# Kernel optimization log

Measured on AMD Instinct MI355X. Metric: run time of the kernel, lower is better.

## Reference

```python
import jax, jax.numpy as jnp
import numpy as np

B, C, S = 32, 256, 64  # batch, channels, spatial_size (h == w == S)


def _xavier(key, shape):
    fan_in, fan_out = shape[0], shape[1]
    bound = float(np.sqrt(6.0 / (fan_in + fan_out)))
    return jax.random.uniform(key, shape, jnp.float32, -bound, bound)


def setup_inputs() -> dict:
    key = jax.random.key(0)
    ks = jax.random.split(key, 7)
    x = jax.random.normal(ks[0], (B, C, S, S), dtype=jnp.float32)
    ww0 = _xavier(ks[1], (S, 1))
    ww1 = _xavier(ks[2], (S, 1))
    ww2 = _xavier(ks[3], (S, 1))
    hw0 = _xavier(ks[4], (S, 1))
    hw1 = _xavier(ks[5], (S, 1))
    hw2 = _xavier(ks[6], (S, 1))
    z = jnp.zeros((1, S), dtype=jnp.float32)
    return {
        'x': x,
        'ww0': ww0, 'ww1': ww1, 'ww2': ww2,
        'wb0': z, 'wb1': z, 'wb2': z,
        'hw0': hw0, 'hw1': hw1, 'hw2': hw2,
        'hb0': z, 'hb1': z, 'hb2': z,
    }


def _branch(mean_vec, max_vec, w0, w1, w2, b0, b1, b2):
    # mean_vec, max_vec: (b, S); w*: (S, 1); b*: (1, S)
    s = jax.nn.softmax(mean_vec, axis=1)          # (b, S)
    y0 = mean_vec @ w0                            # (b, 1)
    y1 = max_vec @ w1                             # (b, 1)
    y0_t = jnp.tanh(y0 * s + b0)                  # (b, S)
    y1_t = jnp.tanh(y1 * s + b1)                  # (b, S)
    return (y1_t @ w2) * y0_t + b2                # (b, S)


def reference(x, ww0, ww1, ww2, wb0, wb1, wb2, hw0, hw1, hw2, hb0, hb1, hb2):
    # x: (b, c, h, w) with h == w == S
    sp_max = jnp.max(x, axis=1)                   # (b, h, w)
    sp_mean = jnp.mean(x, axis=1)                 # (b, h, w)
    width_max = jnp.max(sp_max, axis=1)           # (b, w)
    width_mean = jnp.mean(sp_mean, axis=1)        # (b, w)
    height_max = jnp.max(sp_max, axis=2)          # (b, h)
    height_mean = jnp.mean(sp_mean, axis=2)       # (b, h)
    y_w = _branch(width_mean, width_max, ww0, ww1, ww2, wb0, wb1, wb2)   # (b, w)
    y_h = _branch(height_mean, height_max, hw0, hw1, hw2, hb0, hb1, hb2)  # (b, h)
    spatial = jnp.tanh(y_h[:, :, None] * y_w[:, None, :])[:, None]       # (b,1,h,w)
    return x * (spatial + 1.0)
```

## Files before the change

kernel.cpp:

```cpp
#include <hip/hip_runtime.h>
#include <float.h>

#define BB 32
#define CC 256
#define SS 64
#define IMG (SS * SS)
#define NPIX (BB * IMG)
#define NTOT (BB * CC * IMG)

__device__ __forceinline__ float4 f4max(float4 a, float4 b) {
    return make_float4(fmaxf(a.x, b.x), fmaxf(a.y, b.y), fmaxf(a.z, b.z), fmaxf(a.w, b.w));
}
__device__ __forceinline__ float4 f4add(float4 a, float4 b) {
    return make_float4(a.x + b.x, a.y + b.y, a.z + b.z, a.w + b.w);
}

__global__ __launch_bounds__(256) void reduce_c_kernel(const float* __restrict__ x,
                                                       float* __restrict__ sp_max,
                                                       float* __restrict__ sp_mean) {
    const int blk   = blockIdx.x;
    const int b     = blk >> 4;
    const int chunk = blk & 15;
    const int tid   = threadIdx.x;
    const int wave  = tid >> 6;
    const int lane  = tid & 63;
    const int pos   = (chunk << 8) + (lane << 2);

    const float* xp = x + ((size_t)(b * CC + wave * 64) << 12) + pos;

    float4 vmax = make_float4(-FLT_MAX, -FLT_MAX, -FLT_MAX, -FLT_MAX);
    float4 vsum = make_float4(0.f, 0.f, 0.f, 0.f);
#pragma unroll 8
    for (int c = 0; c < 64; ++c) {
        float4 v = *(const float4*)(xp + ((size_t)c << 12));
        vmax = f4max(vmax, v);
        vsum = f4add(vsum, v);
    }

    __shared__ float4 smax[4][64];
    __shared__ float4 ssum[4][64];
    smax[wave][lane] = vmax;
    ssum[wave][lane] = vsum;
    __syncthreads();

    if (wave == 0) {
        float4 m = smax[0][lane];
        float4 s = ssum[0][lane];
#pragma unroll
        for (int w = 1; w < 4; ++w) {
            m = f4max(m, smax[w][lane]);
            s = f4add(s, ssum[w][lane]);
        }
        const float inv = 1.0f / (float)CC;
        float4 mn = make_float4(s.x * inv, s.y * inv, s.z * inv, s.w * inv);
        *(float4*)(sp_max + (size_t)b * IMG + pos) = m;
        *(float4*)(sp_mean + (size_t)b * IMG + pos) = mn;
    }
}

__device__ __forceinline__ float allreduce_sum(float v) {
#pragma unroll
    for (int o = 32; o > 0; o >>= 1) v += __shfl_xor(v, o);
    return v;
}
__device__ __forceinline__ float allreduce_max(float v) {
#pragma unroll
    for (int o = 32; o > 0; o >>= 1) v = fmaxf(v, __shfl_xor(v, o));
    return v;
}

__device__ __forceinline__ float branch_lane(float meanv, float maxv,
                                             float w0, float w1, float w2,
                                             float b0, float b1, float b2) {
    float m  = allreduce_max(meanv);
    float e  = expf(meanv - m);
    float s  = e / allreduce_sum(e);
    float y0 = allreduce_sum(meanv * w0);
    float y1 = allreduce_sum(maxv * w1);
    float y0t = tanhf(fmaf(y0, s, b0));
    float y1t = tanhf(fmaf(y1, s, b1));
    float yw2 = allreduce_sum(y1t * w2);
    return fmaf(yw2, y0t, b2);
}

__global__ __launch_bounds__(64) void branch_kernel(
        const float* __restrict__ sp_max, const float* __restrict__ sp_mean,
        const float* __restrict__ ww0, const float* __restrict__ ww1, const float* __restrict__ ww2,
        const float* __restrict__ wb0, const float* __restrict__ wb1, const float* __restrict__ wb2,
        const float* __restrict__ hw0, const float* __restrict__ hw1, const float* __restrict__ hw2,
        const float* __restrict__ hb0, const float* __restrict__ hb1, const float* __restrict__ hb2,
        float* __restrict__ spatial) {
    const int b = blockIdx.x;
    const int t = threadIdx.x;
    const float* smx = sp_max + (size_t)b * IMG;
    const float* smn = sp_mean + (size_t)b * IMG;

    float wmax = -FLT_MAX, wsum = 0.f;
    float hmax = -FLT_MAX, hsum = 0.f;
#pragma unroll 4
    for (int i = 0; i < 64; ++i) {
        wmax = fmaxf(wmax, smx[i * 64 + t]);
        wsum += smn[i * 64 + t];
        hmax = fmaxf(hmax, smx[t * 64 + i]);
        hsum += smn[t * 64 + i];
    }
    const float inv = 1.0f / (float)SS;
    float y_w = branch_lane(wsum * inv, wmax, ww0[t], ww1[t], ww2[t], wb0[t], wb1[t], wb2[t]);
    float y_h = branch_lane(hsum * inv, hmax, hw0[t], hw1[t], hw2[t], hb0[t], hb1[t], hb2[t]);

    __shared__ float sh_h[64];
    sh_h[t] = y_h;
    __syncthreads();

    float* sp = spatial + (size_t)b * IMG;
#pragma unroll 4
    for (int h = 0; h < 64; ++h) {
        sp[h * 64 + t] = tanhf(sh_h[h] * y_w);
    }
}

__global__ __launch_bounds__(256) void apply_kernel(const float* __restrict__ x,
                                                    const float* __restrict__ spatial,
                                                    float* __restrict__ out) {
    const int n4 = NTOT / 4;
    const int stride = gridDim.x * blockDim.x;
    for (int i = blockIdx.x * blockDim.x + threadIdx.x; i < n4; i += stride) {
        const size_t base = (size_t)i << 2;
        float4 xv = ((const float4*)x)[i];
        const size_t b   = base >> 20;
        const size_t pos = base & (IMG - 1);
        float4 sv = *(const float4*)(spatial + (b << 12) + pos);
        float4 ov = make_float4(xv.x * (sv.x + 1.0f), xv.y * (sv.y + 1.0f),
                                xv.z * (sv.z + 1.0f), xv.w * (sv.w + 1.0f));
        ((float4*)out)[i] = ov;
    }
}

extern "C" void kernel_launch(void* const* d_in, const int* in_sizes, int n_in,
                              void* d_out, int out_size, void* d_ws, size_t ws_size,
                              hipStream_t stream) {
    const float* x   = (const float*)d_in[0];
    const float* ww0 = (const float*)d_in[1];
    const float* ww1 = (const float*)d_in[2];
    const float* ww2 = (const float*)d_in[3];
    const float* wb0 = (const float*)d_in[4];
    const float* wb1 = (const float*)d_in[5];
    const float* wb2 = (const float*)d_in[6];
    const float* hw0 = (const float*)d_in[7];
    const float* hw1 = (const float*)d_in[8];
    const float* hw2 = (const float*)d_in[9];
    const float* hb0 = (const float*)d_in[10];
    const float* hb1 = (const float*)d_in[11];
    const float* hb2 = (const float*)d_in[12];
    float* out = (float*)d_out;

    float* sp_max  = (float*)d_ws;
    float* sp_mean = sp_max + NPIX;
    float* spatial = sp_mean + NPIX;

    reduce_c_kernel<<<NPIX / 256, 256, 0, stream>>>(x, sp_max, sp_mean);
    branch_kernel<<<BB, 64, 0, stream>>>(sp_max, sp_mean,
                                         ww0, ww1, ww2, wb0, wb1, wb2,
                                         hw0, hw1, hw2, hb0, hb1, hb2, spatial);
    apply_kernel<<<2048, 256, 0, stream>>>(x, spatial, out);
}
```

Baseline: 79.82 us.

## Use native vector types, nontemporal output stores, deeper unroll, larger apply grid

Replaces float4 with clang ext_vector_type arithmetic, raises the channel-reduction unroll from 8 to 16, writes the output with nontemporal stores, and doubles the apply kernel grid. The nontemporal stores aim to keep the large output stream from evicting cached data such as x and the spatial map. The other changes are meant to raise memory-level parallelism in these bandwidth-bound kernels. The cost is possible extra register pressure from the deeper unroll and more blocks to schedule.

```diff
diff --git a/kernel.cpp b/kernel.cpp
--- a/kernel.cpp
+++ b/kernel.cpp
@@ -8,11 +8,13 @@
 #define NPIX (BB * IMG)
 #define NTOT (BB * CC * IMG)
 
-__device__ __forceinline__ float4 f4max(float4 a, float4 b) {
-    return make_float4(fmaxf(a.x, b.x), fmaxf(a.y, b.y), fmaxf(a.z, b.z), fmaxf(a.w, b.w));
-}
-__device__ __forceinline__ float4 f4add(float4 a, float4 b) {
-    return make_float4(a.x + b.x, a.y + b.y, a.z + b.z, a.w + b.w);
+typedef float f32x4 __attribute__((ext_vector_type(4)));
+
+__device__ __forceinline__ f32x4 f4max(f32x4 a, f32x4 b) {
+    f32x4 r;
+    r.x = fmaxf(a.x, b.x); r.y = fmaxf(a.y, b.y);
+    r.z = fmaxf(a.z, b.z); r.w = fmaxf(a.w, b.w);
+    return r;
 }
 
 __global__ __launch_bounds__(256) void reduce_c_kernel(const float* __restrict__ x,
@@ -28,33 +30,33 @@
 
     const float* xp = x + ((size_t)(b * CC + wave * 64) << 12) + pos;
 
-    float4 vmax = make_float4(-FLT_MAX, -FLT_MAX, -FLT_MAX, -FLT_MAX);
-    float4 vsum = make_float4(0.f, 0.f, 0.f, 0.f);
-#pragma unroll 8
+    f32x4 vmax = (f32x4)(-FLT_MAX);
+    f32x4 vsum = (f32x4)(0.f);
+#pragma unroll 16
     for (int c = 0; c < 64; ++c) {
-        float4 v = *(const float4*)(xp + ((size_t)c << 12));
+        f32x4 v = *(const f32x4*)(xp + ((size_t)c << 12));
         vmax = f4max(vmax, v);
-        vsum = f4add(vsum, v);
+        vsum += v;
     }
 
-    __shared__ float4 smax[4][64];
-    __shared__ float4 ssum[4][64];
+    __shared__ f32x4 smax[4][64];
+    __shared__ f32x4 ssum[4][64];
     smax[wave][lane] = vmax;
     ssum[wave][lane] = vsum;
     __syncthreads();
 
     if (wave == 0) {
-        float4 m = smax[0][lane];
-        float4 s = ssum[0][lane];
+        f32x4 m = smax[0][lane];
+        f32x4 s = ssum[0][lane];
 #pragma unroll
         for (int w = 1; w < 4; ++w) {
             m = f4max(m, smax[w][lane]);
-            s = f4add(s, ssum[w][lane]);
+            s += ssum[w][lane];
         }
         const float inv = 1.0f / (float)CC;
-        float4 mn = make_float4(s.x * inv, s.y * inv, s.z * inv, s.w * inv);
-        *(float4*)(sp_max + (size_t)b * IMG + pos) = m;
-        *(float4*)(sp_mean + (size_t)b * IMG + pos) = mn;
+        f32x4 mn = s * inv;
+        *(f32x4*)(sp_max + (size_t)b * IMG + pos) = m;
+        *(f32x4*)(sp_mean + (size_t)b * IMG + pos) = mn;
     }
 }
 
@@ -126,13 +128,12 @@
     const int stride = gridDim.x * blockDim.x;
     for (int i = blockIdx.x * blockDim.x + threadIdx.x; i < n4; i += stride) {
         const size_t base = (size_t)i << 2;
-        float4 xv = ((const float4*)x)[i];
+        f32x4 xv = ((const f32x4*)x)[i];
         const size_t b   = base >> 20;
         const size_t pos = base & (IMG - 1);
-        float4 sv = *(const float4*)(spatial + (b << 12) + pos);
-        float4 ov = make_float4(xv.x * (sv.x + 1.0f), xv.y * (sv.y + 1.0f),
-                                xv.z * (sv.z + 1.0f), xv.w * (sv.w + 1.0f));
-        ((float4*)out)[i] = ov;
+        f32x4 sv = *(const f32x4*)(spatial + (b << 12) + pos);
+        f32x4 ov = xv * (sv + 1.0f);
+        __builtin_nontemporal_store(ov, ((f32x4*)out) + i);
     }
 }
 
@@ -162,5 +163,5 @@
     branch_kernel<<<BB, 64, 0, stream>>>(sp_max, sp_mean,
                                          ww0, ww1, ww2, wb0, wb1, wb2,
                                          hw0, hw1, hw2, hb0, hb1, hb2, spatial);
-    apply_kernel<<<2048, 256, 0, stream>>>(x, spatial, out);
+    apply_kernel<<<4096, 256, 0, stream>>>(x, spatial, out);
 }
```

Measured after the change: 78.57 us. About the same (-1.6%).
